# Performance work log

Hardware: AMD Instinct MI355X
Metric: run time of the kernel (lower is better)

## Reference

```python
import jax, jax.numpy as jnp
import numpy as np
import math

N, L, D = 1024, 32, 768
N_OUT, IN_DIM, OUT_DIM = 16, 64, 64
EPS = 1e-8


def setup_inputs() -> dict:
    key = jax.random.key(0)
    ks = jax.random.split(key, 4)
    x = jax.random.normal(ks[0], (N, L, D), jnp.float32)
    mask = jnp.ones((N, L), jnp.float32)
    scaled = lambda k, shape, fan: jax.random.normal(k, shape, jnp.float32) * (1.0 / np.sqrt(fan).astype(np.float32))
    Wscore = scaled(ks[1], (L, D, 1), D)
    Bscore = jnp.zeros((L, 1, 1), jnp.float32)
    Wcap = scaled(ks[2], (L, D, IN_DIM), D)
    Bcap = jnp.zeros((L, 1, IN_DIM), jnp.float32)
    Wvote = scaled(ks[3], (L, N_OUT, IN_DIM, OUT_DIM), IN_DIM)
    Bvote = jnp.zeros((L, N_OUT, 1, OUT_DIM), jnp.float32)
    beta_use = jnp.zeros((L, 1, 1, 1), jnp.float32)
    beta_ign = jnp.zeros((1, N_OUT, 1, 1), jnp.float32)
    return dict(x=x, mask=mask, Wscore=Wscore, Bscore=Bscore, Wcap=Wcap,
                Bcap=Bcap, Wvote=Wvote, Bvote=Bvote, beta_use=beta_use,
                beta_ign=beta_ign, iters=3)


def reference(x, mask, Wscore, Bscore, Wcap, Bcap, Wvote, Bvote, beta_use, beta_ign, iters):
    n_out = Wvote.shape[1]
    half_pi = np.float32(0.5 * math.pi)
    x_t = jnp.transpose(x, (1, 0, 2))                      # [L, N, D]
    a_in = jnp.matmul(x_t, Wscore) + Bscore                # [L, N, 1]
    mu_in = jax.nn.gelu(jnp.matmul(x_t, Wcap) + Bcap, approximate=False)  # [L, N, in_dim]
    f_a_in = jax.nn.sigmoid(a_in) * jnp.transpose(mask)[..., None]        # [L, N, 1]
    f_a_in = f_a_in[:, None, :, :]                         # [L, 1, N, 1]
    # votes: [L, n_out, N, out_dim] (einsum avoids materializing repeated mu_in)
    V = jnp.einsum('lni,lkio->lkno', mu_in, Wvote) + Bvote

    R = jnp.full((1, n_out, 1, 1), 1.0 / n_out, dtype=x.dtype)
    a_out = mu_out = var_out = None
    for t in range(iters):
        if t > 0:
            log_p = (-jnp.sum((V - mu_out[None]) ** 2 / (2.0 * var_out[None] + EPS), axis=-1)
                     - 1.0 - half_pi
                     - 0.5 * jnp.sum(jnp.log(var_out[None] + EPS), axis=-1))   # [L, n_out, N]
            R = jax.nn.softmax(jax.nn.log_sigmoid(a_out)[None] + log_p[..., None], axis=1)
        D_use = f_a_in * R                                  # [L, n_out, N, 1]
        D_ign = f_a_in - D_use
        a_out = jnp.sum(beta_use * D_use, axis=0) - jnp.sum(beta_ign * D_ign, axis=0)  # [n_out, N, 1]
        denom = jnp.sum(D_use, axis=0) + EPS                # [n_out, N, 1]
        mu_out = jnp.sum(D_use * V, axis=0) / denom         # [n_out, N, out_dim]
        var_out = jnp.sum(D_use * (V - mu_out[None]) ** 2, axis=0) / denom

    a_fin = jnp.transpose(a_out[..., 0])                    # [N, n_out]
    mu_fin = jnp.transpose(mu_out, (1, 0, 2))               # [N, n_out, out_dim]
    return a_fin, mu_fin
```

## Files before the change

### kernel.cpp

```cpp
#include <hip/hip_runtime.h>
#include <hip/hip_bf16.h>

#define L_DIM 32
#define N_DIM 1024
#define D_DIM 768
#define K_DIM 16
#define I_DIM 64
#define O_DIM 64
#define EPSF 1e-8f
#define PX 72

typedef unsigned short u16;
typedef __attribute__((ext_vector_type(8))) short short8;
typedef __attribute__((ext_vector_type(4))) float f32x4;
#define MFMA __builtin_amdgcn_mfma_f32_16x16x32_bf16

__device__ __forceinline__ float bf2f(u16 v) {
    union { unsigned int u; float f; } x; x.u = ((unsigned int)v) << 16; return x.f;
}
__device__ __forceinline__ u16 f2bf(float f) {
    union { float f; unsigned int u; } x; x.f = f;
    unsigned int u = x.u;
    u += 0x7FFFu + ((u >> 16) & 1u);
    return (u16)(u >> 16);
}
__device__ __forceinline__ void split2(float v, u16& h, u16& l) {
    u16 hh = f2bf(v);
    h = hh;
    l = f2bf(v - bf2f(hh));
}
__device__ __forceinline__ void store_split4(u16* ph, u16* pl, float4 v) {
    unsigned u0 = __float_as_uint(v.x), u1 = __float_as_uint(v.y);
    unsigned u2 = __float_as_uint(v.z), u3 = __float_as_uint(v.w);
    uint2 H, L;
    H.x = (u0 >> 16) | (u1 & 0xFFFF0000u);
    H.y = (u2 >> 16) | (u3 & 0xFFFF0000u);
    float l0 = v.x - __uint_as_float(u0 & 0xFFFF0000u);
    float l1 = v.y - __uint_as_float(u1 & 0xFFFF0000u);
    float l2 = v.z - __uint_as_float(u2 & 0xFFFF0000u);
    float l3 = v.w - __uint_as_float(u3 & 0xFFFF0000u);
    L.x = (__float_as_uint(l0) >> 16) | (__float_as_uint(l1) & 0xFFFF0000u);
    L.y = (__float_as_uint(l2) >> 16) | (__float_as_uint(l3) & 0xFFFF0000u);
    *(uint2*)ph = H;
    *(uint2*)pl = L;
}

__global__ __launch_bounds__(256) void prep_wcap(
    const float* __restrict__ W, u16* __restrict__ H, u16* __restrict__ Lo)
{
    const int l = blockIdx.y, d0 = blockIdx.x * 64, t = threadIdx.x;
    __shared__ float tile[64][65];
    #pragma unroll
    for (int p = 0; p < 4; p++) {
        int dd = p * 16 + (t >> 4), i4 = (t & 15) * 4;
        float4 v = *(const float4*)&W[((size_t)l * D_DIM + d0 + dd) * I_DIM + i4];
        tile[dd][i4] = v.x; tile[dd][i4+1] = v.y; tile[dd][i4+2] = v.z; tile[dd][i4+3] = v.w;
    }
    __syncthreads();
    #pragma unroll
    for (int p = 0; p < 4; p++) {
        int i = p * 16 + (t >> 4), dd0 = (t & 15) * 4;
        u16 h[4], lo[4];
        #pragma unroll
        for (int j = 0; j < 4; j++) split2(tile[dd0 + j][i], h[j], lo[j]);
        size_t base = ((size_t)l * I_DIM + i) * D_DIM + d0 + dd0;
        uint2 ph; ph.x = h[0] | ((unsigned)h[1] << 16); ph.y = h[2] | ((unsigned)h[3] << 16);
        uint2 pl; pl.x = lo[0] | ((unsigned)lo[1] << 16); pl.y = lo[2] | ((unsigned)lo[3] << 16);
        *(uint2*)&H[base] = ph;
        *(uint2*)&Lo[base] = pl;
    }
}

__global__ __launch_bounds__(256) void prep_wvote(
    const float* __restrict__ W, u16* __restrict__ H, u16* __restrict__ Lo)
{
    const int l = blockIdx.y, k = blockIdx.x, t = threadIdx.x;
    __shared__ float tile[64][65];
    #pragma unroll
    for (int p = 0; p < 4; p++) {
        int i = p * 16 + (t >> 4), o4 = (t & 15) * 4;
        float4 v = *(const float4*)&W[(((size_t)l * K_DIM + k) * I_DIM + i) * O_DIM + o4];
        tile[i][o4] = v.x; tile[i][o4+1] = v.y; tile[i][o4+2] = v.z; tile[i][o4+3] = v.w;
    }
    __syncthreads();
    #pragma unroll
    for (int p = 0; p < 4; p++) {
        int o = p * 16 + (t >> 4), i0 = (t & 15) * 4;
        u16 h[4], lo[4];
        #pragma unroll
        for (int j = 0; j < 4; j++) split2(tile[i0 + j][o], h[j], lo[j]);
        size_t base = (((size_t)l * K_DIM + k) * O_DIM + o) * I_DIM + i0;
        uint2 ph; ph.x = h[0] | ((unsigned)h[1] << 16); ph.y = h[2] | ((unsigned)h[3] << 16);
        uint2 pl; pl.x = lo[0] | ((unsigned)lo[1] << 16); pl.y = lo[2] | ((unsigned)lo[3] << 16);
        *(uint2*)&H[base] = ph;
        *(uint2*)&Lo[base] = pl;
    }
}

#define A_CHUNK(K0, R0, R1, WH0, WL0, WH1, WL1, BUF)                        \
  {                                                                          \
    const float* wp = &wsc_s[(K0) + sd];                                     \
    fa0 += R0.x * wp[0] + R0.y * wp[1] + R0.z * wp[2] + R0.w * wp[3];        \
    fa1 += R1.x * wp[0] + R1.y * wp[1] + R1.z * wp[2] + R1.w * wp[3];        \
    store_split4(&xh[BUF][sg][sd],      &xl[BUF][sg][sd],      R0);          \
    store_split4(&xh[BUF][16 + sg][sd], &xl[BUF][16 + sg][sd], R1);          \
    __syncthreads();                                                         \
    if ((K0) + 128 < D_DIM) {                                                \
      R0 = *(const float4*)&x[xoff0 + (K0) + 128 + sd];                      \
      R1 = *(const float4*)&x[xoff1 + (K0) + 128 + sd];                      \
    }                                                                        \
    {                                                                        \
      short8 bh, bl;                                                         \
      bh = *(const short8*)&xh[BUF][ln16][quad * 8];                         \
      bl = *(const short8*)&xl[BUF][ln16][quad * 8];                         \
      acc0 = MFMA(WH0, bh, acc0, 0, 0, 0);                                   \
      acc0 = MFMA(WH0, bl, acc0, 0, 0, 0);                                   \
      acc0 = MFMA(WL0, bh, acc0, 0, 0, 0);                                   \
      bh = *(const short8*)&xh[BUF][16 + ln16][quad * 8];                    \
      bl = *(const short8*)&xl[BUF][16 + ln16][quad * 8];                    \
      acc1 = MFMA(WH0, bh, acc1, 0, 0, 0);                                   \
      acc1 = MFMA(WH0, bl, acc1, 0, 0, 0);                                   \
      acc1 = MFMA(WL0, bh, acc1, 0, 0, 0);                                   \
      bh = *(const short8*)&xh[BUF][ln16][32 + quad * 8];                    \
      bl = *(const short8*)&xl[BUF][ln16][32 + quad * 8];                    \
      acc0 = MFMA(WH1, bh, acc0, 0, 0, 0);                                   \
      acc0 = MFMA(WH1, bl, acc0, 0, 0, 0);                                   \
      acc0 = MFMA(WL1, bh, acc0, 0, 0, 0);                                   \
      bh = *(const short8*)&xh[BUF][16 + ln16][32 + quad * 8];               \
      bl = *(const short8*)&xl[BUF][16 + ln16][32 + quad * 8];               \
      acc1 = MFMA(WH1, bh, acc1, 0, 0, 0);                                   \
      acc1 = MFMA(WH1, bl, acc1, 0, 0, 0);                                   \
      acc1 = MFMA(WL1, bh, acc1, 0, 0, 0);                                   \
    }                                                                        \
    if ((K0) + 128 < D_DIM) {                                                \
      WH0 = *(const short8*)&WcH[wrow + (K0) + 128];                         \
      WL0 = *(const short8*)&WcL[wrow + (K0) + 128];                         \
      WH1 = *(const short8*)&WcH[wrow + (K0) + 160];                         \
      WL1 = *(const short8*)&WcL[wrow + (K0) + 160];                         \
    }                                                                        \
  }

__global__ __launch_bounds__(256, 4) void kernelA(
    const float* __restrict__ x, const float* __restrict__ mask,
    const float* __restrict__ Wscore, const float* __restrict__ Bscore,
    const u16* __restrict__ WcH, const u16* __restrict__ WcL,
    const float* __restrict__ Bcap,
    float* __restrict__ mu_out, float* __restrict__ fa_out,
    int nbase, int nchunk)
{
    const int bid  = blockIdx.y * gridDim.x + blockIdx.x;
    const int slot = bid >> 3;
    const int l    = (bid & 7) + 8 * (slot & 3);
    const int n0l  = (slot >> 2) * 32;

    const int t    = threadIdx.x;
    const int w    = t >> 6;
    const int lane = t & 63;
    const int quad = lane >> 4;
    const int ln16 = lane & 15;

    __shared__ u16 xh[2][32][PX], xl[2][32][PX];
    __shared__ float wsc_s[D_DIM];
    __shared__ float bcap_s[64];

    for (int i = t; i < D_DIM; i += 256) wsc_s[i] = Wscore[l * D_DIM + i];
    if (t < 64) bcap_s[t] = Bcap[l * I_DIM + t];

    const int sg = t >> 4;
    const int sd = (t & 15) * 4;

    const size_t xoff0 = ((size_t)(nbase + n0l + sg) * L_DIM + l) * D_DIM;
    const size_t xoff1 = ((size_t)(nbase + n0l + 16 + sg) * L_DIM + l) * D_DIM;

    float4 r0a = *(const float4*)&x[xoff0 + sd];
    float4 r1a = *(const float4*)&x[xoff1 + sd];
    float4 r0b = *(const float4*)&x[xoff0 + 64 + sd];
    float4 r1b = *(const float4*)&x[xoff1 + 64 + sd];

    const size_t wrow = ((size_t)l * I_DIM + (w * 16 + ln16)) * D_DIM + quad * 8;
    short8 wha0 = *(const short8*)&WcH[wrow];
    short8 wla0 = *(const short8*)&WcL[wrow];
    short8 wha1 = *(const short8*)&WcH[wrow + 32];
    short8 wla1 = *(const short8*)&WcL[wrow + 32];
    short8 whb0 = *(const short8*)&WcH[wrow + 64];
    short8 wlb0 = *(const short8*)&WcL[wrow + 64];
    short8 whb1 = *(const short8*)&WcH[wrow + 96];
    short8 wlb1 = *(const short8*)&WcL[wrow + 96];

    __syncthreads();

    f32x4 acc0 = {0.f, 0.f, 0.f, 0.f};
    f32x4 acc1 = {0.f, 0.f, 0.f, 0.f};
    float fa0 = 0.f, fa1 = 0.f;

    #pragma unroll
    for (int cc = 0; cc < 6; cc++) {
        A_CHUNK(cc * 128,      r0a, r1a, wha0, wla0, wha1, wla1, 0)
        A_CHUNK(cc * 128 + 64, r0b, r1b, whb0, wlb0, whb1, wlb1, 1)
    }

    fa0 += __shfl_xor(fa0, 1, 64); fa1 += __shfl_xor(fa1, 1, 64);
    fa0 += __shfl_xor(fa0, 2, 64); fa1 += __shfl_xor(fa1, 2, 64);
    fa0 += __shfl_xor(fa0, 4, 64); fa1 += __shfl_xor(fa1, 4, 64);
    fa0 += __shfl_xor(fa0, 8, 64); fa1 += __shfl_xor(fa1, 8, 64);
    if ((t & 15) == 0) {
        float bs = Bscore[l];
        {
            float a = fa0 + bs;
            float sig = 1.f / (1.f + expf(-a));
            float m = mask[(size_t)(nbase + n0l + sg) * L_DIM + l];
            fa_out[(size_t)l * nchunk + n0l + sg] = sig * m;
        }
        {
            float a = fa1 + bs;
            float sig = 1.f / (1.f + expf(-a));
            float m = mask[(size_t)(nbase + n0l + 16 + sg) * L_DIM + l];
            fa_out[(size_t)l * nchunk + n0l + 16 + sg] = sig * m;
        }
    }

    #pragma unroll
    for (int c = 0; c < 2; c++) {
        const f32x4 a = (c == 0) ? acc0 : acc1;
        const int n = c * 16 + ln16;
        const int i0 = w * 16 + quad * 4;
        float4 o;
        float* op = (float*)&o;
        #pragma unroll
        for (int r = 0; r < 4; r++) {
            float v = a[r] + bcap_s[i0 + r];
            op[r] = 0.5f * v * (1.f + erff(v * 0.70710678118f));
        }
        *(float4*)&mu_out[((size_t)l * nchunk + n0l + n) * I_DIM + i0] = o;
    }
}

__global__ __launch_bounds__(256) void kernelB(
    const float* __restrict__ mu_in,
    const u16* __restrict__ WvH, const u16* __restrict__ WvL,
    const float* __restrict__ Bvote,
    float* __restrict__ V, int nchunk)
{
    const int bid  = (blockIdx.z * gridDim.y + blockIdx.y) * gridDim.x + blockIdx.x;
    const int slot = bid >> 3;
    const int l    = (bid & 7) + 8 * (slot & 3);
    const int rem  = slot >> 2;
    const int k    = rem & 15;
    const int n0l  = (rem >> 4) * 64;

    const int t    = threadIdx.x;
    const int w    = t >> 6;
    const int lane = t & 63;
    const int quad = lane >> 4;
    const int ln16 = lane & 15;

    __shared__ u16 mh[64][PX], ml[64][PX];
    __shared__ float bvote_s[64];

    const int srow = t >> 4, scol = (t & 15) * 4;
    float4 m0 = *(const float4*)&mu_in[((size_t)l * nchunk + n0l + srow) * I_DIM + scol];
    float4 m1 = *(const float4*)&mu_in[((size_t)l * nchunk + n0l + 16 + srow) * I_DIM + scol];
    float4 m2 = *(const float4*)&mu_in[((size_t)l * nchunk + n0l + 32 + srow) * I_DIM + scol];
    float4 m3 = *(const float4*)&mu_in[((size_t)l * nchunk + n0l + 48 + srow) * I_DIM + scol];

    const size_t wrow = (((size_t)l * K_DIM + k) * O_DIM + (w * 16 + ln16)) * I_DIM + quad * 8;
    short8 ah0 = *(const short8*)&WvH[wrow];
    short8 al0 = *(const short8*)&WvL[wrow];
    short8 ah1 = *(const short8*)&WvH[wrow + 32];
    short8 al1 = *(const short8*)&WvL[wrow + 32];

    if (t < 64) bvote_s[t] = Bvote[((size_t)l * K_DIM + k) * O_DIM + t];

    store_split4(&mh[srow][scol],      &ml[srow][scol],      m0);
    store_split4(&mh[16 + srow][scol], &ml[16 + srow][scol], m1);
    store_split4(&mh[32 + srow][scol], &ml[32 + srow][scol], m2);
    store_split4(&mh[48 + srow][scol], &ml[48 + srow][scol], m3);
    __syncthreads();

    f32x4 acc[4] = {{0.f,0.f,0.f,0.f},{0.f,0.f,0.f,0.f},{0.f,0.f,0.f,0.f},{0.f,0.f,0.f,0.f}};

    #pragma unroll
    for (int c = 0; c < 4; c++) {
        const int n = c * 16 + ln16;
        short8 bh = *(const short8*)&mh[n][quad * 8];
        short8 bl = *(const short8*)&ml[n][quad * 8];
        acc[c] = MFMA(ah0, bh, acc[c], 0, 0, 0);
        acc[c] = MFMA(ah0, bl, acc[c], 0, 0, 0);
        acc[c] = MFMA(al0, bh, acc[c], 0, 0, 0);
    }
    #pragma unroll
    for (int c = 0; c < 4; c++) {
        const int n = c * 16 + ln16;
        short8 bh = *(const short8*)&mh[n][32 + quad * 8];
        short8 bl = *(const short8*)&ml[n][32 + quad * 8];
        acc[c] = MFMA(ah1, bh, acc[c], 0, 0, 0);
        acc[c] = MFMA(ah1, bl, acc[c], 0, 0, 0);
        acc[c] = MFMA(al1, bh, acc[c], 0, 0, 0);
    }

    #pragma unroll
    for (int c = 0; c < 4; c++) {
        const int n = c * 16 + ln16;
        const int o0 = w * 16 + quad * 4;
        float4 o;
        o.x = acc[c][0] + bvote_s[o0];
        o.y = acc[c][1] + bvote_s[o0 + 1];
        o.z = acc[c][2] + bvote_s[o0 + 2];
        o.w = acc[c][3] + bvote_s[o0 + 3];
        *(float4*)&V[(((size_t)l * K_DIM + k) * nchunk + n0l + n) * O_DIM + o0] = o;
    }
}

__global__ __launch_bounds__(512, 4) void kernelC(
    const float* __restrict__ V, const float* __restrict__ fa_in,
    const float* __restrict__ beta_use, const float* __restrict__ beta_ign,
    const int* __restrict__ iters_p,
    float* __restrict__ out, int nbase, int nchunk)
{
    const int nl   = blockIdx.x;
    const int ng   = nbase + nl;
    const int t    = threadIdx.x;
    const int k    = t >> 5;
    const int op   = t & 31;
    const int o0   = op * 2;
    const int lane = t & 63;
    int iters = iters_p[0];
    if (iters < 0 || iters > 16) iters = 3;

    __shared__ float fa_s[32];
    __shared__ float bu_s[32];
    __shared__ float R_s[32][17];
    __shared__ float sc_s[32][17];

    if (t < 32) {
        fa_s[t] = fa_in[(size_t)t * nchunk + nl];
        bu_s[t] = beta_use[t];
    }
    R_s[t >> 4][t & 15] = 1.f / 16.f;
    const float bi_k = beta_ign[k];

    float2 Vr[32];
    #pragma unroll
    for (int l = 0; l < 32; l++)
        Vr[l] = *(const float2*)&V[(((size_t)l * K_DIM + k) * nchunk + nl) * O_DIM + o0];
    __syncthreads();

    float mu0 = 0.f, mu1 = 0.f, var0 = 0.f, var1 = 0.f, a_r = 0.f;

    for (int it = 0; it < iters; it++) {
        if (it > 0) {
            float g0 = 1.f / (2.f * var0 + EPSF);
            float g1 = 1.f / (2.f * var1 + EPSF);
            float lvp = logf(var0 + EPSF) + logf(var1 + EPSF);
            lvp += __shfl_xor(lvp, 1, 64);
            lvp += __shfl_xor(lvp, 2, 64);
            lvp += __shfl_xor(lvp, 4, 64);
            lvp += __shfl_xor(lvp, 8, 64);
            lvp += __shfl_xor(lvp, 16, 64);
            float ls = fminf(a_r, 0.f) - log1pf(expf(-fabsf(a_r)));
            const float cst = ls - 1.f - 1.57079632679f - 0.5f * lvp;

            const bool s16 = (lane & 16) != 0;
            const bool s8  = (lane & 8)  != 0;
            const bool s4  = (lane & 4)  != 0;
            const bool s2  = (lane & 2)  != 0;
            const bool s1  = (lane & 1)  != 0;
            float w16[16];
            #pragma unroll
            for (int j = 0; j < 16; j++) {
                float d0 = Vr[j].x - mu0,      d1 = Vr[j].y - mu1;
                float a  = d0 * d0 * g0 + d1 * d1 * g1;
                float e0 = Vr[j + 16].x - mu0, e1 = Vr[j + 16].y - mu1;
                float b  = e0 * e0 * g0 + e1 * e1 * g1;
                float ta = a + __shfl_xor(a, 16, 64);
                float tb = b + __shfl_xor(b, 16, 64);
                w16[j] = s16 ? tb : ta;
            }
            float w8[8];
            #pragma unroll
            for (int j = 0; j < 8; j++) {
                float ta = w16[j]     + __shfl_xor(w16[j],     8, 64);
                float tb = w16[j + 8] + __shfl_xor(w16[j + 8], 8, 64);
                w8[j] = s8 ? tb : ta;
            }
            float w4[4];
            #pragma unroll
            for (int j = 0; j < 4; j++) {
                float ta = w8[j]     + __shfl_xor(w8[j],     4, 64);
                float tb = w8[j + 4] + __shfl_xor(w8[j + 4], 4, 64);
                w4[j] = s4 ? tb : ta;
            }
            float w2[2];
            #pragma unroll
            for (int j = 0; j < 2; j++) {
                float ta = w4[j]     + __shfl_xor(w4[j],     2, 64);
                float tb = w4[j + 2] + __shfl_xor(w4[j + 2], 2, 64);
                w2[j] = s2 ? tb : ta;
            }
            float ta = w2[0] + __shfl_xor(w2[0], 1, 64);
            float tb = w2[1] + __shfl_xor(w2[1], 1, 64);
            float w1 = s1 ? tb : ta;
            sc_s[lane & 31][k] = cst - w1;
            __syncthreads();

            {
                const int lr = t >> 4;
                const int kk = t & 15;
                float s0 = sc_s[lr][kk];
                float m = s0;
                m = fmaxf(m, __shfl_xor(m, 1, 64));
                m = fmaxf(m, __shfl_xor(m, 2, 64));
                m = fmaxf(m, __shfl_xor(m, 4, 64));
                m = fmaxf(m, __shfl_xor(m, 8, 64));
                float e = expf(s0 - m);
                float sum = e;
                sum += __shfl_xor(sum, 1, 64);
                sum += __shfl_xor(sum, 2, 64);
                sum += __shfl_xor(sum, 4, 64);
                sum += __shfl_xor(sum, 8, 64);
                R_s[lr][kk] = e / sum;
            }
            __syncthreads();
        }
        float denom = EPSF, a_acc = 0.f;
        float mua0 = 0.f, mua1 = 0.f, v2a0 = 0.f, v2a1 = 0.f;
        #pragma unroll
        for (int l = 0; l < 32; l++) {
            float Du = fa_s[l] * R_s[l][k];
            denom += Du;
            a_acc += bu_s[l] * Du - bi_k * (fa_s[l] - Du);
            float dv0 = Du * Vr[l].x;
            float dv1 = Du * Vr[l].y;
            mua0 += dv0;  v2a0 += dv0 * Vr[l].x;
            mua1 += dv1;  v2a1 += dv1 * Vr[l].y;
        }
        float invd = 1.f / denom;
        mu0 = mua0 * invd;
        mu1 = mua1 * invd;
        var0 = fmaxf(v2a0 * invd - mu0 * mu0, 0.f);
        var1 = fmaxf(v2a1 * invd - mu1 * mu1, 0.f);
        a_r = a_acc;
    }

    if (op == 0) out[(size_t)ng * K_DIM + k] = a_r;
    float2 o2; o2.x = mu0; o2.y = mu1;
    *(float2*)&out[(size_t)N_DIM * K_DIM + ((size_t)ng * K_DIM + k) * O_DIM + o0] = o2;
}

extern "C" void kernel_launch(void* const* d_in, const int* in_sizes, int n_in,
                              void* d_out, int out_size, void* d_ws, size_t ws_size,
                              hipStream_t stream) {
    (void)out_size;
    static const int EXP[11] = {25165824, 32768, 24576, 32, 1572864, 64,
                                2097152, 65536, 32, 16, 1};
    int mapi[11];
    bool used[64] = {false};
    for (int s = 0; s < 11; s++) {
        mapi[s] = (s < n_in) ? s : 0;
        for (int j = 0; j < n_in && j < 64; j++) {
            if (!used[j] && in_sizes[j] == EXP[s]) { mapi[s] = j; used[j] = true; break; }
        }
    }
    const float* x        = (const float*)d_in[mapi[0]];
    const float* mask     = (const float*)d_in[mapi[1]];
    const float* Wscore   = (const float*)d_in[mapi[2]];
    const float* Bscore   = (const float*)d_in[mapi[3]];
    const float* Wcap     = (const float*)d_in[mapi[4]];
    const float* Bcap     = (const float*)d_in[mapi[5]];
    const float* Wvote    = (const float*)d_in[mapi[6]];
    const float* Bvote    = (const float*)d_in[mapi[7]];
    const float* beta_use = (const float*)d_in[mapi[8]];
    const float* beta_ign = (const float*)d_in[mapi[9]];
    const int*   iters    = (const int*)d_in[mapi[10]];
    float* out = (float*)d_out;

    const size_t WCAP = (size_t)L_DIM * I_DIM * D_DIM;
    const size_t WVOT = (size_t)L_DIM * K_DIM * O_DIM * I_DIM;
    const size_t WBYTES = 2 * WCAP * 2 + 2 * WVOT * 2;

    int C = 64;
    {
        const int cands[5] = {1024, 512, 256, 128, 64};
        for (int i = 0; i < 5; i++) {
            size_t need = WBYTES + (size_t)cands[i] * (128 + 8192 + 131072);
            if (need <= ws_size) { C = cands[i]; break; }
        }
    }

    char* ws = (char*)d_ws;
    u16* WcH = (u16*)ws;
    u16* WcL = (u16*)(ws + WCAP * 2);
    u16* WvH = (u16*)(ws + WCAP * 4);
    u16* WvL = (u16*)(ws + WCAP * 4 + WVOT * 2);
    char* dyn = ws + WBYTES;
    float* fa = (float*)dyn;
    float* mu = (float*)(dyn + (size_t)128 * C);
    float* V  = (float*)(dyn + (size_t)128 * C + (size_t)8192 * C);

    prep_wcap<<<dim3(12, 32), 256, 0, stream>>>(Wcap, WcH, WcL);
    prep_wvote<<<dim3(16, 32), 256, 0, stream>>>(Wvote, WvH, WvL);

    for (int nbase = 0; nbase < N_DIM; nbase += C) {
        kernelA<<<dim3(C / 32, 32), 256, 0, stream>>>(
            x, mask, Wscore, Bscore, WcH, WcL, Bcap, mu, fa, nbase, C);
        kernelB<<<dim3(C / 64, 16, 32), 256, 0, stream>>>(
            mu, WvH, WvL, Bvote, V, C);
        kernelC<<<dim3(C), 512, 0, stream>>>(
            V, fa, beta_use, beta_ign, iters, out, nbase, C);
    }
}
```

Measured before the change: 267.0 us.

## Relayout V per sample, precompute R*fa weights, merge weight-prep kernels

Kernel B now writes V in [n][l][k][o] order, so each kernelC block reads one contiguous 128KB slab instead of strided rows. kernelC stores R·fa and R·fa·beta_use transposed in shared memory and reads them as float4, and it derives the a_out ignore term algebraically from the denominator. The two weight-prep kernels are merged into one launch. The trade-off is that B's stores become more strided, and the algebraic a_out form may round slightly differently.

```diff
diff --git a/kernel.cpp b/kernel.cpp
--- a/kernel.cpp
+++ b/kernel.cpp
@@ -45,55 +45,54 @@
     *(uint2*)pl = L;
 }
 
-__global__ __launch_bounds__(256) void prep_wcap(
-    const float* __restrict__ W, u16* __restrict__ H, u16* __restrict__ Lo)
+__global__ __launch_bounds__(256) void prep_w(
+    const float* __restrict__ Wc, u16* __restrict__ cH, u16* __restrict__ cL,
+    const float* __restrict__ Wv, u16* __restrict__ vH, u16* __restrict__ vL)
 {
-    const int l = blockIdx.y, d0 = blockIdx.x * 64, t = threadIdx.x;
+    const int l = blockIdx.y, t = threadIdx.x;
     __shared__ float tile[64][65];
-    #pragma unroll
-    for (int p = 0; p < 4; p++) {
-        int dd = p * 16 + (t >> 4), i4 = (t & 15) * 4;
-        float4 v = *(const float4*)&W[((size_t)l * D_DIM + d0 + dd) * I_DIM + i4];
-        tile[dd][i4] = v.x; tile[dd][i4+1] = v.y; tile[dd][i4+2] = v.z; tile[dd][i4+3] = v.w;
-    }
-    __syncthreads();
-    #pragma unroll
-    for (int p = 0; p < 4; p++) {
-        int i = p * 16 + (t >> 4), dd0 = (t & 15) * 4;
-        u16 h[4], lo[4];
+    if (blockIdx.x < 12) {
+        const int d0 = blockIdx.x * 64;
         #pragma unroll
-        for (int j = 0; j < 4; j++) split2(tile[dd0 + j][i], h[j], lo[j]);
-        size_t base = ((size_t)l * I_DIM + i) * D_DIM + d0 + dd0;
-        uint2 ph; ph.x = h[0] | ((unsigned)h[1] << 16); ph.y = h[2] | ((unsigned)h[3] << 16);
-        uint2 pl; pl.x = lo[0] | ((unsigned)lo[1] << 16); pl.y = lo[2] | ((unsigned)lo[3] << 16);
-        *(uint2*)&H[base] = ph;
-        *(uint2*)&Lo[base] = pl;
-    }
-}
-
-__global__ __launch_bounds__(256) void prep_wvote(
-    const float* __restrict__ W, u16* __restrict__ H, u16* __restrict__ Lo)
-{
-    const int l = blockIdx.y, k = blockIdx.x, t = threadIdx.x;
-    __shared__ float tile[64][65];
-    #pragma unroll
-    for (int p = 0; p < 4; p++) {
-        int i = p * 16 + (t >> 4), o4 = (t & 15) * 4;
-        float4 v = *(const float4*)&W[(((size_t)l * K_DIM + k) * I_DIM + i) * O_DIM + o4];
-        tile[i][o4] = v.x; tile[i][o4+1] = v.y; tile[i][o4+2] = v.z; tile[i][o4+3] = v.w;
-    }
-    __syncthreads();
-    #pragma unroll
-    for (int p = 0; p < 4; p++) {
-        int o = p * 16 + (t >> 4), i0 = (t & 15) * 4;
-        u16 h[4], lo[4];
+        for (int p = 0; p < 4; p++) {
+            int dd = p * 16 + (t >> 4), i4 = (t & 15) * 4;
+            float4 v = *(const float4*)&Wc[((size_t)l * D_DIM + d0 + dd) * I_DIM + i4];
+            tile[dd][i4] = v.x; tile[dd][i4+1] = v.y; tile[dd][i4+2] = v.z; tile[dd][i4+3] = v.w;
+        }
+        __syncthreads();
         #pragma unroll
-        for (int j = 0; j < 4; j++) split2(tile[i0 + j][o], h[j], lo[j]);
-        size_t base = (((size_t)l * K_DIM + k) * O_DIM + o) * I_DIM + i0;
-        uint2 ph; ph.x = h[0] | ((unsigned)h[1] << 16); ph.y = h[2] | ((unsigned)h[3] << 16);
-        uint2 pl; pl.x = lo[0] | ((unsigned)lo[1] << 16); pl.y = lo[2] | ((unsigned)lo[3] << 16);
-        *(uint2*)&H[base] = ph;
-        *(uint2*)&Lo[base] = pl;
+        for (int p = 0; p < 4; p++) {
+            int i = p * 16 + (t >> 4), dd0 = (t & 15) * 4;
+            u16 h[4], lo[4];
+            #pragma unroll
+            for (int j = 0; j < 4; j++) split2(tile[dd0 + j][i], h[j], lo[j]);
+            size_t base = ((size_t)l * I_DIM + i) * D_DIM + d0 + dd0;
+            uint2 ph; ph.x = h[0] | ((unsigned)h[1] << 16); ph.y = h[2] | ((unsigned)h[3] << 16);
+            uint2 pl; pl.x = lo[0] | ((unsigned)lo[1] << 16); pl.y = lo[2] | ((unsigned)lo[3] << 16);
+            *(uint2*)&cH[base] = ph;
+            *(uint2*)&cL[base] = pl;
+        }
+    } else {
+        const int k = blockIdx.x - 12;
+        #pragma unroll
+        for (int p = 0; p < 4; p++) {
+            int i = p * 16 + (t >> 4), o4 = (t & 15) * 4;
+            float4 v = *(const float4*)&Wv[(((size_t)l * K_DIM + k) * I_DIM + i) * O_DIM + o4];
+            tile[i][o4] = v.x; tile[i][o4+1] = v.y; tile[i][o4+2] = v.z; tile[i][o4+3] = v.w;
+        }
+        __syncthreads();
+        #pragma unroll
+        for (int p = 0; p < 4; p++) {
+            int o = p * 16 + (t >> 4), i0 = (t & 15) * 4;
+            u16 h[4], lo[4];
+            #pragma unroll
+            for (int j = 0; j < 4; j++) split2(tile[i0 + j][o], h[j], lo[j]);
+            size_t base = (((size_t)l * K_DIM + k) * O_DIM + o) * I_DIM + i0;
+            uint2 ph; ph.x = h[0] | ((unsigned)h[1] << 16); ph.y = h[2] | ((unsigned)h[3] << 16);
+            uint2 pl; pl.x = lo[0] | ((unsigned)lo[1] << 16); pl.y = lo[2] | ((unsigned)lo[3] << 16);
+            *(uint2*)&vH[base] = ph;
+            *(uint2*)&vL[base] = pl;
+        }
     }
 }
 
@@ -307,7 +306,7 @@
         o.y = acc[c][1] + bvote_s[o0 + 1];
         o.z = acc[c][2] + bvote_s[o0 + 2];
         o.w = acc[c][3] + bvote_s[o0 + 3];
-        *(float4*)&V[(((size_t)l * K_DIM + k) * nchunk + n0l + n) * O_DIM + o0] = o;
+        *(float4*)&V[(((size_t)(n0l + n) * L_DIM + l) * K_DIM + k) * O_DIM + o0] = o;
     }
 }
 
@@ -327,25 +326,28 @@
     int iters = iters_p[0];
     if (iters < 0 || iters > 16) iters = 3;
 
-    __shared__ float fa_s[32];
-    __shared__ float bu_s[32];
-    __shared__ float R_s[32][17];
     __shared__ float sc_s[32][17];
-
-    if (t < 32) {
-        fa_s[t] = fa_in[(size_t)t * nchunk + nl];
-        bu_s[t] = beta_use[t];
-    }
-    R_s[t >> 4][t & 15] = 1.f / 16.f;
-    const float bi_k = beta_ign[k];
-
+    __shared__ float Rfa_s[16][36];
+    __shared__ float RfaBu_s[16][36];
+
+    const float* Vb = &V[(size_t)nl * (L_DIM * K_DIM * O_DIM)];
     float2 Vr[32];
     #pragma unroll
     for (int l = 0; l < 32; l++)
-        Vr[l] = *(const float2*)&V[(((size_t)l * K_DIM + k) * nchunk + nl) * O_DIM + o0];
+        Vr[l] = *(const float2*)&Vb[(l * K_DIM + k) * O_DIM + o0];
+
+    const int lrow = t >> 4;
+    const int kcol = t & 15;
+    const float fa_l = fa_in[(size_t)lrow * nchunk + nl];
+    const float bu_l = beta_use[lrow];
+    const float bi_k = beta_ign[k];
+
+    Rfa_s[kcol][lrow]   = fa_l * (1.f / 16.f);
+    RfaBu_s[kcol][lrow] = fa_l * bu_l * (1.f / 16.f);
     __syncthreads();
 
     float mu0 = 0.f, mu1 = 0.f, var0 = 0.f, var1 = 0.f, a_r = 0.f;
+    float Sfa = 0.f;
 
     for (int it = 0; it < iters; it++) {
         if (it > 0) {
@@ -404,9 +406,7 @@
             __syncthreads();
 
             {
-                const int lr = t >> 4;
-                const int kk = t & 15;
-                float s0 = sc_s[lr][kk];
+                float s0 = sc_s[lrow][kcol];
                 float m = s0;
                 m = fmaxf(m, __shfl_xor(m, 1, 64));
                 m = fmaxf(m, __shfl_xor(m, 2, 64));
@@ -418,28 +418,40 @@
                 sum += __shfl_xor(sum, 2, 64);
                 sum += __shfl_xor(sum, 4, 64);
                 sum += __shfl_xor(sum, 8, 64);
-                R_s[lr][kk] = e / sum;
+                float R = e / sum;
+                float rf = R * fa_l;
+                Rfa_s[kcol][lrow]   = rf;
+                RfaBu_s[kcol][lrow] = rf * bu_l;
             }
             __syncthreads();
         }
-        float denom = EPSF, a_acc = 0.f;
+        float denom = EPSF, sbu = 0.f;
         float mua0 = 0.f, mua1 = 0.f, v2a0 = 0.f, v2a1 = 0.f;
         #pragma unroll
-        for (int l = 0; l < 32; l++) {
-            float Du = fa_s[l] * R_s[l][k];
-            denom += Du;
-            a_acc += bu_s[l] * Du - bi_k * (fa_s[l] - Du);
-            float dv0 = Du * Vr[l].x;
-            float dv1 = Du * Vr[l].y;
-            mua0 += dv0;  v2a0 += dv0 * Vr[l].x;
-            mua1 += dv1;  v2a1 += dv1 * Vr[l].y;
-        }
+        for (int l4 = 0; l4 < 8; l4++) {
+            const float4 rf = *(const float4*)&Rfa_s[k][l4 * 4];
+            const float4 rb = *(const float4*)&RfaBu_s[k][l4 * 4];
+            const float* rfp = (const float*)&rf;
+            const float* rbp = (const float*)&rb;
+            #pragma unroll
+            for (int j = 0; j < 4; j++) {
+                const int l = l4 * 4 + j;
+                float Du = rfp[j];
+                denom += Du;
+                sbu   += rbp[j];
+                float dv0 = Du * Vr[l].x;
+                float dv1 = Du * Vr[l].y;
+                mua0 += dv0;  v2a0 += dv0 * Vr[l].x;
+                mua1 += dv1;  v2a1 += dv1 * Vr[l].y;
+            }
+        }
+        if (it == 0) Sfa = (denom - EPSF) * 16.f;
+        a_r = sbu + bi_k * ((denom - EPSF) - Sfa);
         float invd = 1.f / denom;
         mu0 = mua0 * invd;
         mu1 = mua1 * invd;
         var0 = fmaxf(v2a0 * invd - mu0 * mu0, 0.f);
         var1 = fmaxf(v2a1 * invd - mu1 * mu1, 0.f);
-        a_r = a_acc;
     }
 
     if (op == 0) out[(size_t)ng * K_DIM + k] = a_r;
@@ -497,8 +509,7 @@
     float* mu = (float*)(dyn + (size_t)128 * C);
     float* V  = (float*)(dyn + (size_t)128 * C + (size_t)8192 * C);
 
-    prep_wcap<<<dim3(12, 32), 256, 0, stream>>>(Wcap, WcH, WcL);
-    prep_wvote<<<dim3(16, 32), 256, 0, stream>>>(Wvote, WvH, WvL);
+    prep_w<<<dim3(28, 32), 256, 0, stream>>>(Wcap, WcH, WcL, Wvote, WvH, WvL);
 
     for (int nbase = 0; nbase < N_DIM; nbase += C) {
         kernelA<<<dim3(C / 32, 32), 256, 0, stream>>>(
```

Result: slower. 304.5 us (+14.0%).
